# Performance work log

Measured on AMD Instinct MI355X. Metric: run time of the kernel, lower is better.

Reference implementation:

```python
import jax, jax.numpy as jnp
import numpy as np

D_MODEL = 3072
N_HEADS = 24
MAX_LEN = 2048
ROPE_THETA = 10000.0
DH = D_MODEL // N_HEADS                  # 128
Q_PROJ = D_MODEL // 2                    # 1536
KV_PROJ = 2 * D_MODEL // 3               # 2048
NOPE = DH // 2                           # 64
ROPE = DH // 2                           # 64
EPS = 1e-5


def layernorm(x, w, b):
    m = jnp.mean(x, axis=-1, keepdims=True)
    v = jnp.mean(jnp.square(x - m), axis=-1, keepdims=True)
    return (x - m) / jnp.sqrt(v + EPS) * w + b


def rotate_half(x):
    h = x.shape[-1] // 2
    return jnp.concatenate([-x[..., h:], x[..., :h]], axis=-1)


def rope_tables(S):
    freqs = 1.0 / ROPE_THETA ** (jnp.arange(0, DH, 2, dtype=jnp.float32) / DH)  # [DH/2]
    emb = jnp.arange(S, dtype=jnp.float32)[:, None] * freqs[None, :]            # [S, DH/2]
    # torch: take first ROPE//2 freqs then .repeat(...,2) => tile along last axis
    cos = jnp.tile(jnp.cos(emb)[:, : ROPE // 2], (1, 2))  # [S, ROPE]
    sin = jnp.tile(jnp.sin(emb)[:, : ROPE // 2], (1, 2))
    return cos[None, None], sin[None, None]               # [1,1,S,ROPE]


def setup_inputs() -> dict:
    key = jax.random.key(0)
    ks = jax.random.split(key, 7)
    x = jax.random.normal(ks[0], (2, 2048, D_MODEL), dtype=jnp.float32)
    p = lambda k, shp: 0.01 * jax.random.normal(k, shp, dtype=jnp.float32)
    return {
        "x": x,
        "W_dq": p(ks[1], (D_MODEL, Q_PROJ)),
        "W_uq": p(ks[2], (Q_PROJ, D_MODEL)),
        "q_ln_w": jnp.ones((Q_PROJ,), jnp.float32),
        "q_ln_b": jnp.zeros((Q_PROJ,), jnp.float32),
        "W_dkv": p(ks[3], (D_MODEL, KV_PROJ + ROPE)),
        "W_ukv": p(ks[4], (KV_PROJ, D_MODEL + N_HEADS * NOPE)),
        "kv_ln_w": jnp.ones((KV_PROJ,), jnp.float32),
        "kv_ln_b": jnp.zeros((KV_PROJ,), jnp.float32),
        "W_o": p(ks[5], (D_MODEL, D_MODEL)),
    }


def reference(x, W_dq, W_uq, q_ln_w, q_ln_b, W_dkv, W_ukv, kv_ln_w, kv_ln_b, W_o):
    B, S, D = x.shape
    cos, sin = rope_tables(S)  # past_length=0, S_full=S

    # Q path: low-rank down/up projection
    cq = layernorm(x @ W_dq, q_ln_w, q_ln_b)          # [B,S,Q_PROJ]
    Q = (cq @ W_uq).reshape(B, S, N_HEADS, DH).transpose(0, 2, 1, 3)  # [B,H,S,DH]
    Q_nope, Q_rope = Q[..., :NOPE], Q[..., NOPE:]
    Q_rope = Q_rope * cos + rotate_half(Q_rope) * sin

    # KV path
    compressed_kv = x @ W_dkv                          # [B,S,KV_PROJ+ROPE]
    KV_lora = layernorm(compressed_kv[..., :KV_PROJ], kv_ln_w, kv_ln_b)
    K_rope = compressed_kv[..., KV_PROJ:]              # [B,S,ROPE]
    KV = (KV_lora @ W_ukv).reshape(B, S, N_HEADS, DH + NOPE).transpose(0, 2, 1, 3)
    K_nope, V = KV[..., :NOPE], KV[..., NOPE:]         # [B,H,S,NOPE], [B,H,S,DH]

    K_rope = K_rope[:, None]                           # [B,1,S,ROPE] shared head
    K_rope = K_rope * cos + rotate_half(K_rope) * sin

    q = jnp.concatenate([Q_nope, Q_rope], axis=-1)     # [B,H,S,DH]
    # k = cat(K_nope, K_rope broadcast over heads)
    k = jnp.concatenate([K_nope, jnp.broadcast_to(K_rope, (B, N_HEADS, S, ROPE))], axis=-1)

    scale = 1.0 / jnp.sqrt(jnp.float32(DH))
    scores = jnp.einsum("bhqd,bhkd->bhqk", q, k) * scale
    causal = jnp.tril(jnp.ones((S, S), dtype=bool))
    scores = jnp.where(causal[None, None], scores, jnp.float32(-jnp.inf))
    attn = jax.nn.softmax(scores, axis=-1)
    out = jnp.einsum("bhqk,bhkd->bhqd", attn, V)
    out = out.transpose(0, 2, 1, 3).reshape(B, S, D)
    out = out @ W_o.T
    return out, compressed_kv
```

## Files before the change

### kernel.cpp

```cpp
#include <hip/hip_runtime.h>

typedef unsigned short u16;
typedef __attribute__((ext_vector_type(8))) short short8;
typedef __attribute__((ext_vector_type(4))) float f32x4;

#define NROWS   4096
#define S_LEN   2048
#define NHEADS  24
#define DMODEL  3072
#define QPROJ   1536
#define KVPROJ  2048
#define CKV_W   2112
#define UKV_N   4608

__device__ __forceinline__ float bf2f(u16 v) {
    unsigned u = ((unsigned)v) << 16; float f; __builtin_memcpy(&f, &u, 4); return f;
}
__device__ __forceinline__ u16 f2bf(float f) {
    unsigned u; __builtin_memcpy(&u, &f, 4);
    u = (u + 0x7FFFu + ((u >> 16) & 1u)) >> 16; return (u16)u;
}
__device__ __forceinline__ u16 f2bf_trunc(float f) {
    unsigned u; __builtin_memcpy(&u, &f, 4);
    return (u16)(u >> 16);
}
__device__ __forceinline__ void async16(const u16* g, u16* l) {
    __builtin_amdgcn_global_load_lds((const __attribute__((address_space(1))) unsigned int*)g,
                                     (__attribute__((address_space(3))) unsigned int*)l,
                                     16, 0, 0);
}

__global__ void conv_bf16(const float* __restrict__ X, u16* __restrict__ Y, int n) {
    int i = (blockIdx.x * 256 + threadIdx.x) * 4;
    if (i >= n) return;
    float4 v = *(const float4*)(X + i);
    Y[i+0] = f2bf(v.x); Y[i+1] = f2bf(v.y); Y[i+2] = f2bf(v.z); Y[i+3] = f2bf(v.w);
}

__global__ void transpose_bf16(const float* __restrict__ W, u16* __restrict__ WT,
                               int K, int N, float scale) {
    __shared__ float t[32][33];
    int nb = blockIdx.x * 32, kb = blockIdx.y * 32;
    int c = threadIdx.x & 31, rq = threadIdx.x >> 5;
#pragma unroll
    for (int i = 0; i < 4; ++i) {
        int r = rq * 4 + i;
        t[r][c] = W[(size_t)(kb + r) * N + nb + c];
    }
    __syncthreads();
#pragma unroll
    for (int i = 0; i < 4; ++i) {
        int r = rq * 4 + i;
        WT[(size_t)(nb + r) * K + kb + c] = f2bf(t[c][r] * scale);
    }
}

__global__ __launch_bounds__(256) void ln_kernel(const float* __restrict__ X, int ldx,
                                                 const float* __restrict__ g,
                                                 const float* __restrict__ b,
                                                 u16* __restrict__ Y, int W) {
    int row = blockIdx.x;
    const float4* x4 = (const float4*)(X + (size_t)row * ldx);
    int W4 = W >> 2;
    float s = 0.f, s2 = 0.f;
    for (int i = threadIdx.x; i < W4; i += 256) {
        float4 v = x4[i];
        s += v.x + v.y + v.z + v.w;
        s2 += v.x * v.x + v.y * v.y + v.z * v.z + v.w * v.w;
    }
#pragma unroll
    for (int off = 32; off >= 1; off >>= 1) { s += __shfl_xor(s, off); s2 += __shfl_xor(s2, off); }
    __shared__ float red[8];
    int w = threadIdx.x >> 6;
    if ((threadIdx.x & 63) == 0) { red[w] = s; red[4 + w] = s2; }
    __syncthreads();
    s  = red[0] + red[1] + red[2] + red[3];
    s2 = red[4] + red[5] + red[6] + red[7];
    float mean = s / W;
    float var  = s2 / W - mean * mean;
    float rstd = rsqrtf(var + 1e-5f);
    const float4* g4 = (const float4*)g;
    const float4* b4 = (const float4*)b;
    u16* y = Y + (size_t)row * W;
    for (int i = threadIdx.x; i < W4; i += 256) {
        float4 v = x4[i], gg = g4[i], bb = b4[i];
        u16 o[4];
        o[0] = f2bf((v.x - mean) * rstd * gg.x + bb.x);
        o[1] = f2bf((v.y - mean) * rstd * gg.y + bb.y);
        o[2] = f2bf((v.z - mean) * rstd * gg.z + bb.z);
        o[3] = f2bf((v.w - mean) * rstd * gg.w + bb.w);
        *(ulong1*)&y[i * 4] = *(ulong1*)o;
    }
}

__global__ __launch_bounds__(256) void ln_bf16_kernel(const u16* __restrict__ X,
                                                      const float* __restrict__ g,
                                                      const float* __restrict__ b,
                                                      u16* __restrict__ Y, int W) {
    int row = blockIdx.x;
    const u16* x = X + (size_t)row * W;
    int W4 = W >> 2;
    float s = 0.f, s2 = 0.f;
    for (int i = threadIdx.x; i < W4; i += 256) {
        ushort4 v = *(const ushort4*)(x + i * 4);
        float a0 = bf2f(v.x), a1 = bf2f(v.y), a2 = bf2f(v.z), a3 = bf2f(v.w);
        s += a0 + a1 + a2 + a3;
        s2 += a0 * a0 + a1 * a1 + a2 * a2 + a3 * a3;
    }
#pragma unroll
    for (int off = 32; off >= 1; off >>= 1) { s += __shfl_xor(s, off); s2 += __shfl_xor(s2, off); }
    __shared__ float red[8];
    int w = threadIdx.x >> 6;
    if ((threadIdx.x & 63) == 0) { red[w] = s; red[4 + w] = s2; }
    __syncthreads();
    s  = red[0] + red[1] + red[2] + red[3];
    s2 = red[4] + red[5] + red[6] + red[7];
    float mean = s / W;
    float var  = s2 / W - mean * mean;
    float rstd = rsqrtf(var + 1e-5f);
    const float4* g4 = (const float4*)g;
    const float4* b4 = (const float4*)b;
    u16* y = Y + (size_t)row * W;
    for (int i = threadIdx.x; i < W4; i += 256) {
        ushort4 v = *(const ushort4*)(x + i * 4);
        float4 gg = g4[i], bb = b4[i];
        u16 o[4];
        o[0] = f2bf((bf2f(v.x) - mean) * rstd * gg.x + bb.x);
        o[1] = f2bf((bf2f(v.y) - mean) * rstd * gg.y + bb.y);
        o[2] = f2bf((bf2f(v.z) - mean) * rstd * gg.z + bb.z);
        o[3] = f2bf((bf2f(v.w) - mean) * rstd * gg.w + bb.w);
        *(ulong1*)&y[i * 4] = *(ulong1*)o;
    }
}

__global__ void rope_k_kernel(const float* __restrict__ ckv, u16* __restrict__ kr) {
    int idx = blockIdx.x * 256 + threadIdx.x;
    int j = idx & 31; int row = idx >> 5;
    int s = row & (S_LEN - 1);
    float freq = __expf(-(float)j * (9.210340371976184f / 64.f));
    float ang = (float)s * freq;
    float c = cosf(ang), si = sinf(ang);
    const float* src = ckv + (size_t)row * CKV_W + KVPROJ;
    float x1 = src[j], x2 = src[j + 32];
    kr[(size_t)row * 64 + j]      = f2bf(x1 * c - x2 * si);
    kr[(size_t)row * 64 + j + 32] = f2bf(x2 * c + x1 * si);
}

template<int MODE>
__global__ __launch_bounds__(256) void gemm_nt(const u16* __restrict__ A,
                                               const u16* __restrict__ B,
                                               void* __restrict__ Cv,
                                               u16* __restrict__ Kn,
                                               u16* __restrict__ Vt,
                                               int M, int N, int K, int nx) {
    __shared__ u16 a_lds[2][128][32];
    __shared__ u16 b_lds[2][128][32];
    int nwg = (int)gridDim.x;
    int bid = (int)blockIdx.x;
    int wg = (bid & 7) * (nwg >> 3) + (bid >> 3);
    int by = wg / nx, bx = wg - by * nx;
    int m0 = by * 128, n0 = bx * 128;
    int tid = threadIdx.x, lane = tid & 63, w = tid >> 6;
    int wm = w >> 1, wn = w & 1;
    int srow = lane >> 2;
    int kx = (lane >> 4) & 2;
    int scol = ((lane & 3) ^ kx) * 8;
    int r0 = w * 32 + srow, r1 = w * 32 + 16 + srow;
    const u16* A0 = A + (size_t)(m0 + r0) * K + scol;
    const u16* A1 = A + (size_t)(m0 + r1) * K + scol;
    int bn0 = n0 + r0; if (bn0 >= N) bn0 = N - 1;
    int bn1 = n0 + r1; if (bn1 >= N) bn1 = N - 1;
    const u16* B0 = B + (size_t)bn0 * K + scol;
    const u16* B1 = B + (size_t)bn1 * K + scol;
    char* aB = (char*)&a_lds[0][0][0];
    char* bB = (char*)&b_lds[0][0][0];
    int d0 = w * 2048, d1 = w * 2048 + 1024;
    int cb = ((lane >> 4) * 16) ^ ((lane & 8) << 2);

    f32x4 acc[4][4] = {};
    async16(A0, (u16*)(aB + d0)); async16(A1, (u16*)(aB + d1));
    async16(B0, (u16*)(bB + d0)); async16(B1, (u16*)(bB + d1));
    __syncthreads();
    int buf = 0;
    for (int kb = 0; kb < K; kb += 32) {
        if (kb + 32 < K) {
            int ob = (buf ^ 1) * 8192;
            async16(A0 + kb + 32, (u16*)(aB + ob + d0));
            async16(A1 + kb + 32, (u16*)(aB + ob + d1));
            async16(B0 + kb + 32, (u16*)(bB + ob + d0));
            async16(B1 + kb + 32, (u16*)(bB + ob + d1));
        }
        const char* ab = aB + buf * 8192;
        const char* bb = bB + buf * 8192;
        short8 af[4], bf[4];
#pragma unroll
        for (int i = 0; i < 4; ++i) {
            af[i] = *(const short8*)(ab + (wm * 64 + i * 16 + (lane & 15)) * 64 + cb);
            bf[i] = *(const short8*)(bb + (wn * 64 + i * 16 + (lane & 15)) * 64 + cb);
        }
#pragma unroll
        for (int i = 0; i < 4; ++i)
#pragma unroll
            for (int j = 0; j < 4; ++j)
                acc[i][j] = __builtin_amdgcn_mfma_f32_16x16x32_bf16(af[i], bf[j], acc[i][j], 0, 0, 0);
        __syncthreads();
        buf ^= 1;
    }

    if (MODE == 2 && wn == 1) {
#pragma unroll
        for (int i = 0; i < 4; ++i) {
            int rowg = m0 + wm * 64 + i * 16 + ((lane >> 4) << 2);
#pragma unroll
            for (int j = 0; j < 2; ++j) {
                int jf = j * 16 + (lane & 15);
                float freq = __expf(-(float)jf * (9.210340371976184f / 64.f));
#pragma unroll
                for (int r = 0; r < 4; ++r) {
                    int s = (rowg + r) & (S_LEN - 1);
                    float ang = (float)s * freq;
                    float cs, sn;
                    __sincosf(ang, &sn, &cs);
                    float x1 = acc[i][j][r], x2 = acc[i][j + 2][r];
                    acc[i][j][r]     = x1 * cs - x2 * sn;
                    acc[i][j + 2][r] = x2 * cs + x1 * sn;
                }
            }
        }
    }

    if (MODE == 3) {
#pragma unroll
        for (int i = 0; i < 4; ++i) {
            int rowg = m0 + wm * 64 + i * 16 + ((lane >> 4) << 2);
            int bb = rowg >> 11;
            int s0 = rowg & (S_LEN - 1);
#pragma unroll
            for (int j = 0; j < 4; ++j) {
                int colbase = n0 + wn * 64 + j * 16;
                int h = colbase / 192;
                int c = colbase - h * 192 + (lane & 15);
                int bh = bb * NHEADS + h;
                if (c < 64) {
#pragma unroll
                    for (int r = 0; r < 4; ++r)
                        Kn[((size_t)bh * S_LEN + s0 + r) * 64 + c] = f2bf(acc[i][j][r]);
                } else {
                    size_t vb = ((size_t)bh * 128 + (c - 64)) * S_LEN + s0;
                    u16 o[4];
#pragma unroll
                    for (int r = 0; r < 4; ++r) o[r] = f2bf(acc[i][j][r]);
                    *(ushort4*)&Vt[vb] = *(ushort4*)o;
                }
            }
        }
        return;
    }

#pragma unroll
    for (int i = 0; i < 4; ++i) {
        int row = m0 + wm * 64 + i * 16 + ((lane >> 4) << 2);
#pragma unroll
        for (int j = 0; j < 4; ++j) {
            int col = n0 + wn * 64 + j * 16 + (lane & 15);
            if (col < N) {
#pragma unroll
                for (int r = 0; r < 4; ++r) {
                    if (MODE != 0) ((u16*)Cv)[(size_t)(row + r) * N + col] = f2bf(acc[i][j][r]);
                    else           ((float*)Cv)[(size_t)(row + r) * N + col] = acc[i][j][r];
                }
            }
        }
    }
}

__global__ __launch_bounds__(256) void attn_kernel(const u16* __restrict__ Qb,
                                                   const u16* __restrict__ Kn,
                                                   const u16* __restrict__ kr_,
                                                   const u16* __restrict__ Vt,
                                                   u16* __restrict__ AO) {
    __shared__ u16 k_lds[64][128];
    __shared__ u16 v_lds[128][64];
    __shared__ u16 p_lds[4][16][64];
    int bid = blockIdx.x;
    int jj = bid >> 3;
    int bh = (bid & 7) * 6 + (jj >> 4);
    int bx = jj & 15;
    int bb = bh / NHEADS, h = bh % NHEADS;
    int tid = threadIdx.x, lane = tid & 63, w = tid >> 6;
    size_t base = (size_t)bb * S_LEN;
    size_t bhS = (size_t)bh * S_LEN;

    const char* Vbyte = (const char*)Vt;
    char* kB = (char*)&k_lds[0][0];
    char* vB = (char*)&v_lds[0][0];
    char* pB = (char*)&p_lds[0][0][0] + w * 2048;
    const char* psrc[4];
    size_t vsrc[4];
    int kd[4];
#pragma unroll
    for (int is = 0; is < 4; ++is) {
        int j = is * 256 + tid;
        int r = j >> 4;
        int p = j & 15;
        int lq = p ^ (r & 7);
        if (lq < 8) psrc[is] = (const char*)Kn  + (bhS  + r) * 128 + lq * 16;
        else        psrc[is] = (const char*)kr_ + (base + r) * 128 + (lq - 8) * 16;
        int d = j >> 3;
        int kbs = (((j & 7) ^ (d & 7)) * 16);
        vsrc[is] = ((size_t)bh * 128 + d) * (S_LEN * 2) + kbs;
        kd[is] = (is * 256 + w * 64) * 16;
    }

    for (int seg = 0; seg < 2; ++seg) {
        int qx = seg == 0 ? (31 - bx) : bx;
        int q0 = qx * 64;

        short8 qf[4];
        {
            int qrow = q0 + w * 16 + (lane & 15);
            const u16* qp = Qb + (base + qrow) * DMODEL + h * 128 + ((lane >> 4) * 8);
#pragma unroll
            for (int ks = 0; ks < 4; ++ks) qf[ks] = *(const short8*)(qp + ks * 32);
        }

        f32x4 acc_o[8] = {};
        float m_run[4], l_run[4];
#pragma unroll
        for (int r = 0; r < 4; ++r) { m_run[r] = -1e30f; l_run[r] = 0.f; }

        int ntiles = qx + 1;
        for (int t = 0; t < ntiles; ++t) {
            size_t kv0 = (size_t)t * 64;
#pragma unroll
            for (int is = 0; is < 4; ++is)
                async16((const u16*)(psrc[is] + kv0 * 128), (u16*)(kB + kd[is]));
#pragma unroll
            for (int is = 0; is < 4; ++is)
                async16((const u16*)(Vbyte + vsrc[is] + kv0 * 2), (u16*)(vB + kd[is]));
            __syncthreads();

            f32x4 sc[4];
            __builtin_amdgcn_s_setprio(1);
#pragma unroll
            for (int nb = 0; nb < 4; ++nb) {
                f32x4 a = {};
                int row = nb * 16 + (lane & 15);
                const char* kb_ = kB + row * 256;
                int x = (row & 7) << 4;
#pragma unroll
                for (int ks = 0; ks < 4; ++ks) {
                    short8 kf = *(const short8*)(kb_ + ((ks * 64 + (lane >> 4) * 16) ^ x));
                    a = __builtin_amdgcn_mfma_f32_16x16x32_bf16(qf[ks], kf, a, 0, 0, 0);
                }
                sc[nb] = a;
            }
            __builtin_amdgcn_s_setprio(0);

            if (t == qx) {
                int kvb = t * 64;
                int qg = q0 + w * 16 + ((lane >> 4) << 2);
#pragma unroll
                for (int nb = 0; nb < 4; ++nb) {
                    int kc = kvb + nb * 16 + (lane & 15);
#pragma unroll
                    for (int r = 0; r < 4; ++r)
                        if (kc > qg + r) sc[nb][r] = -1e30f;
                }
            }
            float rmax[4];
#pragma unroll
            for (int r = 0; r < 4; ++r)
                rmax[r] = fmaxf(fmaxf(sc[0][r], sc[1][r]), fmaxf(sc[2][r], sc[3][r]));
#pragma unroll
            for (int off = 1; off < 16; off <<= 1)
#pragma unroll
                for (int r = 0; r < 4; ++r) rmax[r] = fmaxf(rmax[r], __shfl_xor(rmax[r], off));

            bool ok = (rmax[0] <= m_run[0]) & (rmax[1] <= m_run[1]) &
                      (rmax[2] <= m_run[2]) & (rmax[3] <= m_run[3]);
            if (!__all(ok)) {
                float fac[4];
#pragma unroll
                for (int r = 0; r < 4; ++r) {
                    float mnew = fmaxf(m_run[r], rmax[r]);
                    fac[r] = __expf(m_run[r] - mnew);
                    m_run[r] = mnew;
                    l_run[r] *= fac[r];
                }
#pragma unroll
                for (int db = 0; db < 8; ++db)
#pragma unroll
                    for (int r = 0; r < 4; ++r) acc_o[db][r] *= fac[r];
            }
#pragma unroll
            for (int nb = 0; nb < 4; ++nb)
#pragma unroll
                for (int r = 0; r < 4; ++r) {
                    float p = __expf(sc[nb][r] - m_run[r]);
                    sc[nb][r] = p; l_run[r] += p;
                }

#pragma unroll
            for (int nb = 0; nb < 4; ++nb)
#pragma unroll
                for (int r = 0; r < 4; ++r) {
                    int row = ((lane >> 4) << 2) + r;
                    int cby = (nb * 32 + (lane & 15) * 2) ^ ((row & 7) << 4);
                    *(u16*)(pB + row * 128 + cby) = f2bf_trunc(sc[nb][r]);
                }
            __builtin_amdgcn_sched_barrier(0);
            __builtin_amdgcn_s_setprio(1);
#pragma unroll
            for (int ks = 0; ks < 2; ++ks) {
                int prow = lane & 15;
                short8 pf = *(const short8*)(pB + prow * 128 +
                                ((ks * 64 + (lane >> 4) * 16) ^ ((prow & 7) << 4)));
#pragma unroll
                for (int db = 0; db < 8; ++db) {
                    int row = db * 16 + (lane & 15);
                    const char* vb_ = vB + row * 128;
                    short8 vf = *(const short8*)(vb_ + ((ks * 64 + (lane >> 4) * 16) ^ ((row & 7) << 4)));
                    acc_o[db] = __builtin_amdgcn_mfma_f32_16x16x32_bf16(pf, vf, acc_o[db], 0, 0, 0);
                }
            }
            __builtin_amdgcn_s_setprio(0);
            __syncthreads();
        }

#pragma unroll
        for (int off = 1; off < 16; off <<= 1)
#pragma unroll
            for (int r = 0; r < 4; ++r) l_run[r] += __shfl_xor(l_run[r], off);

        int orow = q0 + w * 16 + ((lane >> 4) << 2);
#pragma unroll
        for (int db = 0; db < 8; ++db)
#pragma unroll
            for (int r = 0; r < 4; ++r) {
                float o = acc_o[db][r] / l_run[r];
                AO[(base + orow + r) * DMODEL + h * 128 + db * 16 + (lane & 15)] = f2bf(o);
            }
    }
}

extern "C" void kernel_launch(void* const* d_in, const int* in_sizes, int n_in,
                              void* d_out, int out_size, void* d_ws, size_t ws_size,
                              hipStream_t stream) {
    (void)in_sizes; (void)n_in; (void)out_size; (void)ws_size;
    const float* x      = (const float*)d_in[0];
    const float* W_dq   = (const float*)d_in[1];
    const float* W_uq   = (const float*)d_in[2];
    const float* q_ln_w = (const float*)d_in[3];
    const float* q_ln_b = (const float*)d_in[4];
    const float* W_dkv  = (const float*)d_in[5];
    const float* W_ukv  = (const float*)d_in[6];
    const float* kv_ln_w= (const float*)d_in[7];
    const float* kv_ln_b= (const float*)d_in[8];
    const float* W_o    = (const float*)d_in[9];

    float* out = (float*)d_out;
    float* ckv = out + (size_t)NROWS * DMODEL;

    char* ws = (char*)d_ws;
    const size_t OFF_WDQT  = 0;
    const size_t OFF_WUQT  = 9437184;
    const size_t OFF_WDKVT = 18874368;
    const size_t OFF_WUKVT = 31850496;
    const size_t OFF_WO    = 50724864;
    const size_t OFF_XB    = 69599232;
    const size_t OFF_QB    = 94765056;
    const size_t OFF_KN    = 119930880;
    const size_t OFF_KR    = 157679616;
    const size_t OFF_SLABA = 158203904;
    const size_t OFF_SLABB = 183369728;
    const size_t OFF_VT    = OFF_XB;

    u16* Wdq_t  = (u16*)(ws + OFF_WDQT);
    u16* Wuq_t  = (u16*)(ws + OFF_WUQT);
    u16* Wdkv_t = (u16*)(ws + OFF_WDKVT);
    u16* Wukv_t = (u16*)(ws + OFF_WUKVT);
    u16* Wo_b   = (u16*)(ws + OFF_WO);
    u16* xb     = (u16*)(ws + OFF_XB);
    u16* qb     = (u16*)(ws + OFF_QB);
    u16* Kn     = (u16*)(ws + OFF_KN);
    u16* kr     = (u16*)(ws + OFF_KR);
    u16* t0b    = (u16*)(ws + OFF_SLABA);
    u16* ao     = (u16*)(ws + OFF_SLABA);
    u16* cq     = (u16*)(ws + OFF_SLABB);
    u16* kvl    = (u16*)(ws + OFF_SLABB);
    u16* Vt     = (u16*)(ws + OFF_VT);

    const float SCALE = 0.08838834764831845f;

    transpose_bf16<<<dim3(QPROJ / 32, DMODEL / 32), 256, 0, stream>>>(W_dq,  Wdq_t,  DMODEL, QPROJ, 1.0f);
    transpose_bf16<<<dim3(DMODEL / 32, QPROJ / 32), 256, 0, stream>>>(W_uq,  Wuq_t,  QPROJ, DMODEL, SCALE);
    transpose_bf16<<<dim3(CKV_W / 32, DMODEL / 32), 256, 0, stream>>>(W_dkv, Wdkv_t, DMODEL, CKV_W, 1.0f);
    transpose_bf16<<<dim3(UKV_N / 32, KVPROJ / 32), 256, 0, stream>>>(W_ukv, Wukv_t, KVPROJ, UKV_N, 1.0f);
    conv_bf16<<<9216, 256, 0, stream>>>(W_o, Wo_b, DMODEL * DMODEL);
    conv_bf16<<<12288, 256, 0, stream>>>(x, xb, NROWS * DMODEL);

    gemm_nt<1><<<(QPROJ / 128) * (NROWS / 128), 256, 0, stream>>>(xb, Wdq_t, t0b, nullptr, nullptr, NROWS, QPROJ, DMODEL, QPROJ / 128);
    ln_bf16_kernel<<<NROWS, 256, 0, stream>>>(t0b, q_ln_w, q_ln_b, cq, QPROJ);
    gemm_nt<2><<<(DMODEL / 128) * (NROWS / 128), 256, 0, stream>>>(cq, Wuq_t, qb, nullptr, nullptr, NROWS, DMODEL, QPROJ, DMODEL / 128);

    gemm_nt<0><<<17 * (NROWS / 128), 256, 0, stream>>>(xb, Wdkv_t, ckv, nullptr, nullptr, NROWS, CKV_W, DMODEL, 17);
    ln_kernel<<<NROWS, 256, 0, stream>>>(ckv, CKV_W, kv_ln_w, kv_ln_b, kvl, KVPROJ);
    rope_k_kernel<<<512, 256, 0, stream>>>(ckv, kr);
    gemm_nt<3><<<(UKV_N / 128) * (NROWS / 128), 256, 0, stream>>>(kvl, Wukv_t, nullptr, Kn, Vt, NROWS, UKV_N, KVPROJ, UKV_N / 128);

    attn_kernel<<<768, 256, 0, stream>>>(qb, Kn, kr, Vt, ao);

    gemm_nt<0><<<(DMODEL / 128) * (NROWS / 128), 256, 0, stream>>>(ao, Wo_b, out, nullptr, nullptr, NROWS, DMODEL, DMODEL, DMODEL / 128);
}
```

Before: 615.0 us.

## Add 128x256-tile GEMM kernel for Q-up, KV-up and output projections

Adds a gemm_big kernel that computes a 128x256 output tile per workgroup, so each wave holds a 64x128 accumulator and reuses every A fragment across 8 B fragments. It also raises wave priority with s_setprio around the MFMA block. The Q-up (with RoPE), KV-up (K/V scatter) and output projection GEMMs use it, while the smaller down-projections keep the 128x128 kernel, which drops its K/V-scatter arguments. The larger tile cuts LDS and global traffic per FLOP but doubles accumulator registers, which can lower occupancy, and halves the grid, which may leave compute units underused.

```diff
diff --git a/kernel.cpp b/kernel.cpp
--- a/kernel.cpp
+++ b/kernel.cpp
@@ -150,8 +150,6 @@
 __global__ __launch_bounds__(256) void gemm_nt(const u16* __restrict__ A,
                                                const u16* __restrict__ B,
                                                void* __restrict__ Cv,
-                                               u16* __restrict__ Kn,
-                                               u16* __restrict__ Vt,
                                                int M, int N, int K, int nx) {
     __shared__ u16 a_lds[2][128][32];
     __shared__ u16 b_lds[2][128][32];
@@ -206,14 +204,104 @@
         __syncthreads();
         buf ^= 1;
     }
-
-    if (MODE == 2 && wn == 1) {
+#pragma unroll
+    for (int i = 0; i < 4; ++i) {
+        int row = m0 + wm * 64 + i * 16 + ((lane >> 4) << 2);
+#pragma unroll
+        for (int j = 0; j < 4; ++j) {
+            int col = n0 + wn * 64 + j * 16 + (lane & 15);
+            if (col < N) {
+#pragma unroll
+                for (int r = 0; r < 4; ++r) {
+                    if (MODE != 0) ((u16*)Cv)[(size_t)(row + r) * N + col] = f2bf(acc[i][j][r]);
+                    else           ((float*)Cv)[(size_t)(row + r) * N + col] = acc[i][j][r];
+                }
+            }
+        }
+    }
+}
+
+template<int MODE>
+__global__ __launch_bounds__(256, 2) void gemm_big(const u16* __restrict__ A,
+                                                   const u16* __restrict__ B,
+                                                   void* __restrict__ Cv,
+                                                   u16* __restrict__ Kn,
+                                                   u16* __restrict__ Vt,
+                                                   int M, int N, int K, int nx) {
+    __shared__ u16 a_lds[2][128][32];
+    __shared__ u16 b_lds[2][256][32];
+    int nwg = (int)gridDim.x;
+    int bid = (int)blockIdx.x;
+    int wg = (bid & 7) * (nwg >> 3) + (bid >> 3);
+    int by = wg / nx, bx = wg - by * nx;
+    int m0 = by * 128, n0 = bx * 256;
+    int tid = threadIdx.x, lane = tid & 63, w = tid >> 6;
+    int wm = w >> 1, wn = w & 1;
+
+    const u16* As[2]; int ad[2];
+#pragma unroll
+    for (int is = 0; is < 2; ++is) {
+        int j = is * 256 + tid;
+        int row = j >> 2;
+        int sc = ((j & 3) ^ (((j >> 5) & 1) << 1)) * 8;
+        As[is] = A + (size_t)(m0 + row) * K + sc;
+        ad[is] = (is * 256 + w * 64) * 16;
+    }
+    const u16* Bs[4]; int bd[4];
+#pragma unroll
+    for (int is = 0; is < 4; ++is) {
+        int j = is * 256 + tid;
+        int row = j >> 2;
+        int sc = ((j & 3) ^ (((j >> 5) & 1) << 1)) * 8;
+        Bs[is] = B + (size_t)(n0 + row) * K + sc;
+        bd[is] = (is * 256 + w * 64) * 16;
+    }
+    char* aB = (char*)&a_lds[0][0][0];
+    char* bB = (char*)&b_lds[0][0][0];
+    int cb = ((lane >> 4) * 16) ^ ((lane & 8) << 2);
+
+    f32x4 acc[4][8] = {};
+#pragma unroll
+    for (int is = 0; is < 2; ++is) async16(As[is], (u16*)(aB + ad[is]));
+#pragma unroll
+    for (int is = 0; is < 4; ++is) async16(Bs[is], (u16*)(bB + bd[is]));
+    __syncthreads();
+    int buf = 0;
+    for (int kb = 0; kb < K; kb += 32) {
+        if (kb + 32 < K) {
+            int oa = (buf ^ 1) * 8192, ob = (buf ^ 1) * 16384;
+#pragma unroll
+            for (int is = 0; is < 2; ++is) async16(As[is] + kb + 32, (u16*)(aB + oa + ad[is]));
+#pragma unroll
+            for (int is = 0; is < 4; ++is) async16(Bs[is] + kb + 32, (u16*)(bB + ob + bd[is]));
+        }
+        const char* ab = aB + buf * 8192;
+        const char* bb = bB + buf * 16384;
+        short8 af[4], bf[8];
+#pragma unroll
+        for (int i = 0; i < 4; ++i)
+            af[i] = *(const short8*)(ab + (wm * 64 + i * 16 + (lane & 15)) * 64 + cb);
+#pragma unroll
+        for (int jn = 0; jn < 8; ++jn)
+            bf[jn] = *(const short8*)(bb + (wn * 128 + jn * 16 + (lane & 15)) * 64 + cb);
+        __builtin_amdgcn_s_setprio(1);
+#pragma unroll
+        for (int i = 0; i < 4; ++i)
+#pragma unroll
+            for (int jn = 0; jn < 8; ++jn)
+                acc[i][jn] = __builtin_amdgcn_mfma_f32_16x16x32_bf16(af[i], bf[jn], acc[i][jn], 0, 0, 0);
+        __builtin_amdgcn_s_setprio(0);
+        __syncthreads();
+        buf ^= 1;
+    }
+
+    if (MODE == 2) {
 #pragma unroll
         for (int i = 0; i < 4; ++i) {
             int rowg = m0 + wm * 64 + i * 16 + ((lane >> 4) << 2);
 #pragma unroll
-            for (int j = 0; j < 2; ++j) {
-                int jf = j * 16 + (lane & 15);
+            for (int jn = 4; jn < 6; ++jn) {
+                int jf = (jn - 4) * 16 + (lane & 15);
                 float freq = __expf(-(float)jf * (9.210340371976184f / 64.f));
 #pragma unroll
                 for (int r = 0; r < 4; ++r) {
@@ -221,9 +309,9 @@
                     float ang = (float)s * freq;
                     float cs, sn;
                     __sincosf(ang, &sn, &cs);
-                    float x1 = acc[i][j][r], x2 = acc[i][j + 2][r];
-                    acc[i][j][r]     = x1 * cs - x2 * sn;
-                    acc[i][j + 2][r] = x2 * cs + x1 * sn;
+                    float x1 = acc[i][jn][r], x2 = acc[i][jn + 2][r];
+                    acc[i][jn][r]     = x1 * cs - x2 * sn;
+                    acc[i][jn + 2][r] = x2 * cs + x1 * sn;
                 }
             }
         }
@@ -233,23 +321,23 @@
 #pragma unroll
         for (int i = 0; i < 4; ++i) {
             int rowg = m0 + wm * 64 + i * 16 + ((lane >> 4) << 2);
-            int bb = rowg >> 11;
+            int bb_ = rowg >> 11;
             int s0 = rowg & (S_LEN - 1);
 #pragma unroll
-            for (int j = 0; j < 4; ++j) {
-                int colbase = n0 + wn * 64 + j * 16;
+            for (int jn = 0; jn < 8; ++jn) {
+                int colbase = n0 + wn * 128 + jn * 16;
                 int h = colbase / 192;
                 int c = colbase - h * 192 + (lane & 15);
-                int bh = bb * NHEADS + h;
+                int bh = bb_ * NHEADS + h;
                 if (c < 64) {
 #pragma unroll
                     for (int r = 0; r < 4; ++r)
-                        Kn[((size_t)bh * S_LEN + s0 + r) * 64 + c] = f2bf(acc[i][j][r]);
+                        Kn[((size_t)bh * S_LEN + s0 + r) * 64 + c] = f2bf(acc[i][jn][r]);
                 } else {
                     size_t vb = ((size_t)bh * 128 + (c - 64)) * S_LEN + s0;
                     u16 o[4];
 #pragma unroll
-                    for (int r = 0; r < 4; ++r) o[r] = f2bf(acc[i][j][r]);
+                    for (int r = 0; r < 4; ++r) o[r] = f2bf(acc[i][jn][r]);
                     *(ushort4*)&Vt[vb] = *(ushort4*)o;
                 }
             }
@@ -261,14 +349,12 @@
     for (int i = 0; i < 4; ++i) {
         int row = m0 + wm * 64 + i * 16 + ((lane >> 4) << 2);
 #pragma unroll
-        for (int j = 0; j < 4; ++j) {
-            int col = n0 + wn * 64 + j * 16 + (lane & 15);
-            if (col < N) {
-#pragma unroll
-                for (int r = 0; r < 4; ++r) {
-                    if (MODE != 0) ((u16*)Cv)[(size_t)(row + r) * N + col] = f2bf(acc[i][j][r]);
-                    else           ((float*)Cv)[(size_t)(row + r) * N + col] = acc[i][j][r];
-                }
+        for (int jn = 0; jn < 8; ++jn) {
+            int col = n0 + wn * 128 + jn * 16 + (lane & 15);
+#pragma unroll
+            for (int r = 0; r < 4; ++r) {
+                if (MODE != 0) ((u16*)Cv)[(size_t)(row + r) * N + col] = f2bf(acc[i][jn][r]);
+                else           ((float*)Cv)[(size_t)(row + r) * N + col] = acc[i][jn][r];
             }
         }
     }
@@ -500,16 +586,16 @@
     conv_bf16<<<9216, 256, 0, stream>>>(W_o, Wo_b, DMODEL * DMODEL);
     conv_bf16<<<12288, 256, 0, stream>>>(x, xb, NROWS * DMODEL);
 
-    gemm_nt<1><<<(QPROJ / 128) * (NROWS / 128), 256, 0, stream>>>(xb, Wdq_t, t0b, nullptr, nullptr, NROWS, QPROJ, DMODEL, QPROJ / 128);
+    gemm_nt<1><<<(QPROJ / 128) * (NROWS / 128), 256, 0, stream>>>(xb, Wdq_t, t0b, NROWS, QPROJ, DMODEL, QPROJ / 128);
     ln_bf16_kernel<<<NROWS, 256, 0, stream>>>(t0b, q_ln_w, q_ln_b, cq, QPROJ);
-    gemm_nt<2><<<(DMODEL / 128) * (NROWS / 128), 256, 0, stream>>>(cq, Wuq_t, qb, nullptr, nullptr, NROWS, DMODEL, QPROJ, DMODEL / 128);
-
-    gemm_nt<0><<<17 * (NROWS / 128), 256, 0, stream>>>(xb, Wdkv_t, ckv, nullptr, nullptr, NROWS, CKV_W, DMODEL, 17);
+    gemm_big<2><<<(NROWS / 128) * (DMODEL / 256), 256, 0, stream>>>(cq, Wuq_t, qb, nullptr, nullptr, NROWS, DMODEL, QPROJ, DMODEL / 256);
+
+    gemm_nt<0><<<17 * (NROWS / 128), 256, 0, stream>>>(xb, Wdkv_t, ckv, NROWS, CKV_W, DMODEL, 17);
     ln_kernel<<<NROWS, 256, 0, stream>>>(ckv, CKV_W, kv_ln_w, kv_ln_b, kvl, KVPROJ);
     rope_k_kernel<<<512, 256, 0, stream>>>(ckv, kr);
-    gemm_nt<3><<<(UKV_N / 128) * (NROWS / 128), 256, 0, stream>>>(kvl, Wukv_t, nullptr, Kn, Vt, NROWS, UKV_N, KVPROJ, UKV_N / 128);
+    gemm_big<3><<<(NROWS / 128) * (UKV_N / 256), 256, 0, stream>>>(kvl, Wukv_t, nullptr, Kn, Vt, NROWS, UKV_N, KVPROJ, UKV_N / 256);
 
     attn_kernel<<<768, 256, 0, stream>>>(qb, Kn, kr, Vt, ao);
 
-    gemm_nt<0><<<(DMODEL / 128) * (NROWS / 128), 256, 0, stream>>>(ao, Wo_b, out, nullptr, nullptr, NROWS, DMODEL, DMODEL, DMODEL / 128);
-}
+    gemm_big<0><<<(NROWS / 128) * (DMODEL / 256), 256, 0, stream>>>(ao, Wo_b, out, nullptr, nullptr, NROWS, DMODEL, DMODEL, DMODEL / 256);
+}
```

Result: slower. 651.4 us (+5.9%).
